# Optimization experiments

Hardware: AMD Instinct MI355X
Metric: run time of the kernel (lower is better)

The kernel has to match this reference:

```python
import jax, jax.numpy as jnp
import numpy as np

B1, B2, N, D = 1, 128, 256, 256
H, C = 8, 32
OUT = 256


def setup_inputs() -> dict:
    key = jax.random.key(0)
    ks = jax.random.split(key, 8)
    in_data = jax.random.normal(ks[0], (B1, B2, N, D), dtype=jnp.float32)
    # binary mask, mostly unmasked
    mask = (jax.random.uniform(ks[1], (B1, B2, N)) > 0.1).astype(jnp.float32)
    nonbatched_bias = jax.random.normal(ks[2], (B1, H, N, N), dtype=jnp.float32)
    scale = 1.0 / np.sqrt(D)
    w_qkv = jax.random.normal(ks[3], (3 * H * C, D), dtype=jnp.float32) * scale  # torch Linear [out,in]
    w_gate = jax.random.normal(ks[4], (H * C, D), dtype=jnp.float32) * scale
    gating_bias = jnp.ones((H * C,), dtype=jnp.float32)
    w_o = jax.random.normal(ks[5], (OUT, H * C), dtype=jnp.float32) * scale
    b_o = jnp.zeros((OUT,), dtype=jnp.float32)
    return {
        "in_data": in_data,
        "mask": mask,
        "nonbatched_bias": nonbatched_bias,
        "w_qkv": w_qkv,
        "w_gate": w_gate,
        "gating_bias": gating_bias,
        "w_o": w_o,
        "b_o": b_o,
    }


def reference(in_data, mask, nonbatched_bias, w_qkv, w_gate, gating_bias, w_o, b_o):
    scaling = C ** (-0.5)
    # fused QKV projection (no bias): [b1,b2,n, 3*h*c]
    qkv = jnp.einsum("xynd,ed->xyne", in_data, w_qkv)
    q, k, v = jnp.split(qkv, 3, axis=-1)

    def heads(t):  # [b1,b2,n,h*c] -> [b1,b2,h,n,c]
        return t.reshape(B1, B2, N, H, C).transpose(0, 1, 3, 2, 4)

    q, k, v = heads(q) * scaling, heads(k), heads(v)
    logits = jnp.einsum("xyhqc,xyhkc->xyhqk", q, k)
    mask_bias = (1e9 * (mask - 1.0))[:, :, None, None, :]  # [b1,b2,1,1,n]
    logits = logits + mask_bias + nonbatched_bias[:, None]  # [b1,b2,h,q,k]
    weights = jax.nn.softmax(logits, axis=-1)
    wa = jnp.einsum("xyhqk,xyhkc->xyhqc", weights, v)
    wa = wa.transpose(0, 1, 3, 2, 4).reshape(B1, B2, N, H * C)
    # sigmoid gating: sigmoid(gate_linear(x) + gating_bias) * weighted_avg
    gate = jax.nn.sigmoid(jnp.einsum("xynd,ed->xyne", in_data, w_gate) + gating_bias)
    wa = gate * wa
    out = jnp.einsum("xyne,oe->xyno", wa, w_o) + b_o
    return out
```

## Files before the change

kernel.cpp:

```cpp
#include <hip/hip_runtime.h>
#include <stdint.h>

#define B2 128
#define NSEQ 256
#define DIM 256
#define NH 8
#define CH 32

typedef __attribute__((ext_vector_type(8))) __bf16 bf16x8;
typedef __attribute__((ext_vector_type(8))) unsigned short u16x8;
typedef __attribute__((ext_vector_type(4))) unsigned short u16x4;
typedef __attribute__((ext_vector_type(4))) unsigned int u32x4;
typedef __attribute__((ext_vector_type(4))) float f32x4;

__device__ __forceinline__ unsigned short f2bf(float f) {
  unsigned int u = __builtin_bit_cast(unsigned int, f);
  u += 0x7FFFu + ((u >> 16) & 1u);
  return (unsigned short)(u >> 16);
}
__device__ __forceinline__ float bf2f(unsigned short h) {
  unsigned int u = ((unsigned int)h) << 16;
  return __builtin_bit_cast(float, u);
}
__device__ __forceinline__ bf16x8 as_bf(u16x8 v) { return __builtin_bit_cast(bf16x8, v); }
__device__ __forceinline__ unsigned int cvtpk(float lo, float hi) {
  unsigned int r;
  asm("v_cvt_pk_bf16_f32 %0, %1, %2" : "=v"(r) : "v"(lo), "v"(hi));
  return r;
}

__device__ __forceinline__ void gload16(void* lds, const void* g) {
  __builtin_amdgcn_global_load_lds(
      (__attribute__((address_space(1))) void*)(g),
      (__attribute__((address_space(3))) void*)(lds), 16, 0, 0);
}

__global__ void k_convert(const float* __restrict__ wqkv, const float* __restrict__ wgate,
                          const float* __restrict__ wo,
                          unsigned short* __restrict__ wallb, unsigned short* __restrict__ wob) {
  const int NWALL = 262144, NWO = 65536;
  int i = blockIdx.x * blockDim.x + threadIdx.x;
  int total4 = (NWALL + NWO) >> 2;
  if (i >= total4) return;
  int e = i << 2;
  float4 v;
  unsigned short* dst;
  if (e < NWALL) {
    v = (e < 196608) ? *reinterpret_cast<const float4*>(wqkv + e)
                     : *reinterpret_cast<const float4*>(wgate + (e - 196608));
    dst = wallb + e;
  } else {
    int o = e - NWALL;
    v = *reinterpret_cast<const float4*>(wo + o);
    dst = wob + o;
  }
  u16x4 r;
  r[0] = f2bf(v.x); r[1] = f2bf(v.y); r[2] = f2bf(v.z); r[3] = f2bf(v.w);
  *reinterpret_cast<u16x4*>(dst) = r;
}

template <int MODE>
__launch_bounds__(256, MODE == 0 ? 3 : 4)
__global__ void k_gemm(const float* __restrict__ Af, const unsigned short* __restrict__ Ab,
                       const unsigned short* __restrict__ Bw,
                       unsigned short* __restrict__ qs, unsigned short* __restrict__ ksb,
                       unsigned short* __restrict__ vsb, unsigned short* __restrict__ gateb,
                       const float* __restrict__ gbias,
                       float* __restrict__ outp, const float* __restrict__ bo) {
  __shared__ __attribute__((aligned(16))) char As[2][MODE == 0 ? 16384 : 8192];
  __shared__ __attribute__((aligned(16))) unsigned short Bs[2][4096];
  const int tid = threadIdx.x, lane = tid & 63, w = tid >> 6;
  const int wr = w >> 1, wc = w & 1;
  const int l15 = lane & 15, hi = lane >> 4;
  const int m0 = blockIdx.x * 128, n0 = blockIdx.y * 128;

  auto stageA = [&](int buf, int k0) {
    if constexpr (MODE == 0) {
#pragma unroll
      for (int q2 = 0; q2 < 4; ++q2) {
        int ob = (w * 4 + q2) * 1024 + (lane << 4);
        int r = ob >> 7, cb = ob & 127;
        int scb = cb ^ ((r & 7) << 4);
        const float* g = Af + (size_t)(m0 + r) * 256 + k0 + (scb >> 2);
        gload16(As[buf] + (size_t)(w * 4 + q2) * 1024, g);
      }
    } else {
#pragma unroll
      for (int q2 = 0; q2 < 2; ++q2) {
        int ob = (w * 2 + q2) * 1024 + (lane << 4);
        int r = ob >> 6, cb = ob & 63;
        int scb = cb ^ ((r & 3) << 4);
        const unsigned short* g = Ab + (size_t)(m0 + r) * 256 + k0 + (scb >> 1);
        gload16(As[buf] + (size_t)(w * 2 + q2) * 1024, g);
      }
    }
  };
  auto stageB = [&](int buf, int k0) {
#pragma unroll
    for (int q2 = 0; q2 < 2; ++q2) {
      int ob = (w * 2 + q2) * 1024 + (lane << 4);
      int r = ob >> 6, cb = ob & 63;
      int scb = cb ^ ((r & 3) << 4);
      const unsigned short* g = Bw + (size_t)(n0 + r) * 256 + k0 + (scb >> 1);
      gload16((char*)Bs[buf] + (size_t)(w * 2 + q2) * 1024, g);
    }
  };

  f32x4 acc[4][4];
#pragma unroll
  for (int i = 0; i < 4; ++i) {
#pragma unroll
    for (int j = 0; j < 4; ++j) acc[i][j] = (f32x4){0.f, 0.f, 0.f, 0.f};
  }

  stageA(0, 0);
  stageB(0, 0);
  asm volatile("s_waitcnt vmcnt(0)" ::: "memory");
  __syncthreads();

#pragma unroll
  for (int kt = 0; kt < 8; ++kt) {
    const int cur = kt & 1;
    if (kt < 7) {
      stageA(cur ^ 1, (kt + 1) * 32);
      stageB(cur ^ 1, (kt + 1) * 32);
    }
    {
      bf16x8 af[4], bfv[4];
#pragma unroll
      for (int fr = 0; fr < 4; ++fr) {
        int ra = wr * 64 + fr * 16 + l15;
        if constexpr (MODE == 0) {
          const char* base = As[cur] + ra * 128;
          int sw = (ra & 7) << 4;
          f32x4 a0 = *reinterpret_cast<const f32x4*>(base + ((hi * 32) ^ sw));
          f32x4 a1 = *reinterpret_cast<const f32x4*>(base + ((hi * 32 + 16) ^ sw));
          u32x4 afu;
          afu[0] = cvtpk(a0[0], a0[1]);
          afu[1] = cvtpk(a0[2], a0[3]);
          afu[2] = cvtpk(a1[0], a1[1]);
          afu[3] = cvtpk(a1[2], a1[3]);
          af[fr] = __builtin_bit_cast(bf16x8, afu);
        } else {
          int off = ra * 64 + ((hi << 4) ^ ((ra & 3) << 4));
          af[fr] = *reinterpret_cast<const bf16x8*>(As[cur] + off);
        }
      }
#pragma unroll
      for (int fc = 0; fc < 4; ++fc) {
        int rb = wc * 64 + fc * 16 + l15;
        int off = rb * 64 + ((hi << 4) ^ ((rb & 3) << 4));
        bfv[fc] = *reinterpret_cast<const bf16x8*>((const char*)Bs[cur] + off);
      }
#pragma unroll
      for (int fr = 0; fr < 4; ++fr) {
#pragma unroll
        for (int fc = 0; fc < 4; ++fc)
          acc[fr][fc] = __builtin_amdgcn_mfma_f32_16x16x32_bf16(af[fr], bfv[fc], acc[fr][fc], 0, 0, 0);
      }
    }
    asm volatile("s_waitcnt vmcnt(0)" ::: "memory");
    __syncthreads();
  }

  if (MODE == 0) {
#pragma unroll
    for (int fr = 0; fr < 4; ++fr) {
      int mrow = m0 + wr * 64 + fr * 16 + (hi << 2);
      int b = mrow >> 8, n = mrow & 255;
#pragma unroll
      for (int fc = 0; fc < 4; ++fc) {
        int e = n0 + wc * 64 + fc * 16 + l15;
        int which = e >> 8, loc = e & 255, hh = loc >> 5, cc = loc & 31;
#pragma unroll
        for (int i = 0; i < 4; ++i) {
          float v = acc[fr][fc][i];
          size_t idx = ((size_t)(b * 8 + hh) * 256 + (n + i)) * 32 + cc;
          if (which == 0) {
            qs[idx] = f2bf(v * 0.17677669529663687f);
          } else if (which == 1) {
            ksb[idx] = f2bf(v);
          } else if (which == 2) {
            vsb[idx] = f2bf(v);
          } else {
            float gsig = 1.0f / (1.0f + __expf(-(v + gbias[loc])));
            gateb[idx] = f2bf(gsig);
          }
        }
      }
    }
  } else {
#pragma unroll
    for (int fr = 0; fr < 4; ++fr) {
      int mrow = m0 + wr * 64 + fr * 16 + (hi << 2);
#pragma unroll
      for (int fc = 0; fc < 4; ++fc) {
        int e = n0 + wc * 64 + fc * 16 + l15;
        float bb = bo[e];
#pragma unroll
        for (int i = 0; i < 4; ++i)
          outp[(size_t)(mrow + i) * 256 + e] = acc[fr][fc][i] + bb;
      }
    }
  }
}

__launch_bounds__(512, 2)
__global__ void k_attn(const unsigned short* __restrict__ qs, const unsigned short* __restrict__ ksb,
                       const unsigned short* __restrict__ vsb, const unsigned short* __restrict__ gateb,
                       const float* __restrict__ mask, const float* __restrict__ nb,
                       unsigned short* __restrict__ wag) {
  __shared__ __attribute__((aligned(16))) unsigned short vt[32][264];
  __shared__ __attribute__((aligned(16))) unsigned short pch[8][16][72];
  __shared__ __attribute__((aligned(16))) unsigned short Kl[16][64][8];
  __shared__ __attribute__((aligned(16))) float mb[256];
  __shared__ float invl[8][16];
  const int tid = threadIdx.x, lane = tid & 63, w = tid >> 6;
  const int l15 = lane & 15, hi = lane >> 4;
  const int b = blockIdx.x, h = blockIdx.y;
  const size_t bh = (size_t)(b * 8 + h);
  const unsigned short* kbase = ksb + bh * 8192;
  const unsigned short* vbase = vsb + bh * 8192;
  const unsigned short* qbase = qs + bh * 8192;
  const float* nbh = nb + (size_t)h * 65536;

  if (tid < 256) {
    mb[tid] = 1e9f * (mask[b * 256 + tid] - 1.0f);
    const unsigned short* vrow = vbase + tid * 32;
#pragma unroll
    for (int c0 = 0; c0 < 32; c0 += 8) {
      u16x8 vv = *reinterpret_cast<const u16x8*>(vrow + c0);
#pragma unroll
      for (int j = 0; j < 8; ++j) vt[c0 + j][tid] = vv[j];
    }
  } else {
    const int key = tid - 256;
    const unsigned short* krow = kbase + key * 32;
#pragma unroll
    for (int c8 = 0; c8 < 4; ++c8)
      *reinterpret_cast<u16x8*>(&Kl[key >> 4][c8 * 16 + (key & 15)][0]) =
          *reinterpret_cast<const u16x8*>(krow + c8 * 8);
  }
  __syncthreads();

  const f32x4 zero = {0.f, 0.f, 0.f, 0.f};
#pragma unroll 1
  for (int fr = 0; fr < 2; ++fr) {
    const int q0 = w * 32 + fr * 16;
    u16x8 qf = *reinterpret_cast<const u16x8*>(qbase + (q0 + l15) * 32 + hi * 8);

    f32x4 sacc[16];
    __builtin_amdgcn_s_setprio(1);
#pragma unroll
    for (int kt = 0; kt < 16; ++kt) {
      bf16x8 kf = *reinterpret_cast<const bf16x8*>(&Kl[kt][lane][0]);
      sacc[kt] = __builtin_amdgcn_mfma_f32_16x16x32_bf16(kf, as_bf(qf), zero, 0, 0, 0);
    }
    __builtin_amdgcn_s_setprio(0);

    const float* nbq = nbh + (size_t)(q0 + l15) * 256;
#pragma unroll
    for (int kt = 0; kt < 16; ++kt) {
      float4 nb4 = *reinterpret_cast<const float4*>(nbq + kt * 16 + hi * 4);
      float4 mb4 = *reinterpret_cast<const float4*>(&mb[kt * 16 + hi * 4]);
      sacc[kt][0] += mb4.x + nb4.x;
      sacc[kt][1] += mb4.y + nb4.y;
      sacc[kt][2] += mb4.z + nb4.z;
      sacc[kt][3] += mb4.w + nb4.w;
    }
    float mx = -3.0e38f;
#pragma unroll
    for (int kt = 0; kt < 16; ++kt) {
#pragma unroll
      for (int i = 0; i < 4; ++i) mx = fmaxf(mx, sacc[kt][i]);
    }
    mx = fmaxf(mx, __shfl_xor(mx, 16));
    mx = fmaxf(mx, __shfl_xor(mx, 32));

    float sum = 0.f;
    f32x4 wacc[2];
    wacc[0] = zero; wacc[1] = zero;
#pragma unroll
    for (int c = 0; c < 4; ++c) {
#pragma unroll
      for (int ktl = 0; ktl < 4; ++ktl) {
        const int kt = c * 4 + ktl;
        u16x4 pv;
#pragma unroll
        for (int i = 0; i < 4; ++i) {
          float p = __expf(sacc[kt][i] - mx);
          sum += p;
          pv[i] = f2bf(p);
        }
        *reinterpret_cast<u16x4*>(&pch[w][l15][ktl * 16 + hi * 4]) = pv;
      }
      asm volatile("s_waitcnt lgkmcnt(0)" ::: "memory");
      __builtin_amdgcn_sched_barrier(0);
      __builtin_amdgcn_s_setprio(1);
#pragma unroll
      for (int ks2 = 0; ks2 < 2; ++ks2) {
        bf16x8 pa = *reinterpret_cast<const bf16x8*>(&pch[w][l15][ks2 * 32 + hi * 8]);
#pragma unroll
        for (int ct = 0; ct < 2; ++ct) {
          bf16x8 vb = *reinterpret_cast<const bf16x8*>(&vt[ct * 16 + l15][c * 64 + ks2 * 32 + hi * 8]);
          wacc[ct] = __builtin_amdgcn_mfma_f32_16x16x32_bf16(pa, vb, wacc[ct], 0, 0, 0);
        }
      }
      __builtin_amdgcn_s_setprio(0);
    }
    sum += __shfl_xor(sum, 16);
    sum += __shfl_xor(sum, 32);
    const float inv = 1.0f / sum;
    if (hi == 0) invl[w][l15] = inv;

    float* et = reinterpret_cast<float*>(&pch[w][0][0]);
#pragma unroll
    for (int ct = 0; ct < 2; ++ct) {
#pragma unroll
      for (int i = 0; i < 4; ++i)
        et[(hi * 4 + i) * 36 + ct * 16 + l15] = wacc[ct][i];
    }
    asm volatile("s_waitcnt lgkmcnt(0)" ::: "memory");
    __builtin_amdgcn_sched_barrier(0);
    const int eq = lane >> 2, eh = lane & 3;
    float4 v0 = *reinterpret_cast<const float4*>(&et[eq * 36 + eh * 8]);
    float4 v1 = *reinterpret_cast<const float4*>(&et[eq * 36 + eh * 8 + 4]);
    const float iv = invl[w][eq];
    const int qrow = q0 + eq;
    u16x8 g = *reinterpret_cast<const u16x8*>(gateb + bh * 8192 + qrow * 32 + eh * 8);
    u16x8 ov;
    ov[0] = f2bf(bf2f(g[0]) * v0.x * iv);
    ov[1] = f2bf(bf2f(g[1]) * v0.y * iv);
    ov[2] = f2bf(bf2f(g[2]) * v0.z * iv);
    ov[3] = f2bf(bf2f(g[3]) * v0.w * iv);
    ov[4] = f2bf(bf2f(g[4]) * v1.x * iv);
    ov[5] = f2bf(bf2f(g[5]) * v1.y * iv);
    ov[6] = f2bf(bf2f(g[6]) * v1.z * iv);
    ov[7] = f2bf(bf2f(g[7]) * v1.w * iv);
    *reinterpret_cast<u16x8*>(wag + ((size_t)(b * 256 + qrow)) * 256 + h * 32 + eh * 8) = ov;
    asm volatile("s_waitcnt lgkmcnt(0)" ::: "memory");
    __builtin_amdgcn_sched_barrier(0);
  }
}

extern "C" void kernel_launch(void* const* d_in, const int* in_sizes, int n_in,
                              void* d_out, int out_size, void* d_ws, size_t ws_size,
                              hipStream_t stream) {
  const float* x     = (const float*)d_in[0];
  const float* mask  = (const float*)d_in[1];
  const float* nb    = (const float*)d_in[2];
  const float* wqkv  = (const float*)d_in[3];
  const float* wgate = (const float*)d_in[4];
  const float* gbias = (const float*)d_in[5];
  const float* wo    = (const float*)d_in[6];
  const float* bo    = (const float*)d_in[7];
  float* outp = (float*)d_out;

  char* ws = (char*)d_ws;
  unsigned short* wag   = (unsigned short*)(ws);
  unsigned short* wallb = (unsigned short*)(ws + 16777216);
  unsigned short* wob   = (unsigned short*)(ws + 17301504);
  unsigned short* qs    = (unsigned short*)(ws + 17432576);
  unsigned short* ksb   = (unsigned short*)(ws + 34209792);
  unsigned short* vsb   = (unsigned short*)(ws + 50987008);
  unsigned short* gateb = (unsigned short*)(ws + 67764224);

  k_convert<<<dim3(320), dim3(256), 0, stream>>>(wqkv, wgate, wo, wallb, wob);
  k_gemm<0><<<dim3(256, 8), dim3(256), 0, stream>>>(x, nullptr, wallb, qs, ksb, vsb, gateb, gbias, nullptr, nullptr);
  k_attn<<<dim3(128, 8), dim3(512), 0, stream>>>(qs, ksb, vsb, gateb, mask, nb, wag);
  k_gemm<1><<<dim3(256, 2), dim3(256), 0, stream>>>(nullptr, wag, wob, nullptr, nullptr, nullptr, nullptr, nullptr, outp, bo);
}
```

Before: 129.0 us.

## Re-swizzle bf16 GEMM LDS tiles by row pairs and move barrier to loop top

The bf16 A and B shared-memory staging now packs two 64-byte rows into each 128-byte line and XORs the 16-byte slot by the row-pair index, so the fragment reads should hit fewer LDS bank conflicts. The fragment load address math is updated to match. The wait-and-barrier now sits at the top of each k-iteration, fenced by sched_barrier, instead of at the end. This is meant to let the prefetch for the next tile be issued right after the barrier. The barrier moves could introduce a race on the double buffer if the ordering is wrong.

Result: faster. 124.5 us (-3.5%).

```diff
diff --git a/kernel.cpp b/kernel.cpp
--- a/kernel.cpp
+++ b/kernel.cpp
@@ -74,6 +74,17 @@
   const int l15 = lane & 15, hi = lane >> 4;
   const int m0 = blockIdx.x * 128, n0 = blockIdx.y * 128;
 
+  auto stage_pair = [&](char* sbuf, const unsigned short* gsrc, int row0, int k0) {
+#pragma unroll
+    for (int q2 = 0; q2 < 2; ++q2) {
+      int i = q2 * 256 + tid;
+      int rp = i >> 3, sp = i & 7;
+      int sl = sp ^ (rp & 7);
+      int row = 2 * rp + (sl >> 2), s3 = sl & 3;
+      const unsigned short* g = gsrc + (size_t)(row0 + row) * 256 + k0 + s3 * 8;
+      gload16(sbuf + q2 * 4096 + w * 1024, g);
+    }
+  };
   auto stageA = [&](int buf, int k0) {
     if constexpr (MODE == 0) {
 #pragma unroll
@@ -85,26 +96,10 @@
         gload16(As[buf] + (size_t)(w * 4 + q2) * 1024, g);
       }
     } else {
-#pragma unroll
-      for (int q2 = 0; q2 < 2; ++q2) {
-        int ob = (w * 2 + q2) * 1024 + (lane << 4);
-        int r = ob >> 6, cb = ob & 63;
-        int scb = cb ^ ((r & 3) << 4);
-        const unsigned short* g = Ab + (size_t)(m0 + r) * 256 + k0 + (scb >> 1);
-        gload16(As[buf] + (size_t)(w * 2 + q2) * 1024, g);
-      }
+      stage_pair(As[buf], Ab, m0, k0);
     }
   };
-  auto stageB = [&](int buf, int k0) {
-#pragma unroll
-    for (int q2 = 0; q2 < 2; ++q2) {
-      int ob = (w * 2 + q2) * 1024 + (lane << 4);
-      int r = ob >> 6, cb = ob & 63;
-      int scb = cb ^ ((r & 3) << 4);
-      const unsigned short* g = Bw + (size_t)(n0 + r) * 256 + k0 + (scb >> 1);
-      gload16((char*)Bs[buf] + (size_t)(w * 2 + q2) * 1024, g);
-    }
-  };
+  auto stageB = [&](int buf, int k0) { stage_pair((char*)Bs[buf], Bw, n0, k0); };
 
   f32x4 acc[4][4];
 #pragma unroll
@@ -115,12 +110,14 @@
 
   stageA(0, 0);
   stageB(0, 0);
-  asm volatile("s_waitcnt vmcnt(0)" ::: "memory");
-  __syncthreads();
 
 #pragma unroll
   for (int kt = 0; kt < 8; ++kt) {
     const int cur = kt & 1;
+    asm volatile("s_waitcnt vmcnt(0)" ::: "memory");
+    __builtin_amdgcn_sched_barrier(0);
+    __builtin_amdgcn_s_barrier();
+    __builtin_amdgcn_sched_barrier(0);
     if (kt < 7) {
       stageA(cur ^ 1, (kt + 1) * 32);
       stageB(cur ^ 1, (kt + 1) * 32);
@@ -142,14 +139,18 @@
           afu[3] = cvtpk(a1[2], a1[3]);
           af[fr] = __builtin_bit_cast(bf16x8, afu);
         } else {
-          int off = ra * 64 + ((hi << 4) ^ ((ra & 3) << 4));
+          int rp = ra >> 1;
+          int sl = ((ra & 1) << 2) | hi;
+          int off = rp * 128 + (sl ^ (rp & 7)) * 16;
           af[fr] = *reinterpret_cast<const bf16x8*>(As[cur] + off);
         }
       }
 #pragma unroll
       for (int fc = 0; fc < 4; ++fc) {
         int rb = wc * 64 + fc * 16 + l15;
-        int off = rb * 64 + ((hi << 4) ^ ((rb & 3) << 4));
+        int rp = rb >> 1;
+        int sl = ((rb & 1) << 2) | hi;
+        int off = rp * 128 + (sl ^ (rp & 7)) * 16;
         bfv[fc] = *reinterpret_cast<const bf16x8*>((const char*)Bs[cur] + off);
       }
 #pragma unroll
@@ -159,8 +160,6 @@
           acc[fr][fc] = __builtin_amdgcn_mfma_f32_16x16x32_bf16(af[fr], bfv[fc], acc[fr][fc], 0, 0, 0);
       }
     }
-    asm volatile("s_waitcnt vmcnt(0)" ::: "memory");
-    __syncthreads();
   }
 
   if (MODE == 0) {
```
